# Kernel tuning notes

Hardware: AMD Instinct MI355X
Metric: run time of the kernel (lower is better)

Reference implementation:

```python
import jax, jax.numpy as jnp
import numpy as np

D_MODEL = 1024
D_FFN = 4096
H = 16
D_HEAD = D_MODEL // H
B, L = 2, 2048
EPS = 1e-6


def layer_norm(x, a, b):
    # Matches torch: std is unbiased (ddof=1), and divides by (std + eps)
    mean = jnp.mean(x, axis=-1, keepdims=True)
    var = jnp.sum((x - mean) ** 2, axis=-1, keepdims=True) / (x.shape[-1] - 1)
    std = jnp.sqrt(var)
    return (x - mean) / (std + EPS) * a + b


def setup_inputs() -> dict:
    key = jax.random.key(0)
    ks = jax.random.split(key, 10)
    s = 0.02
    x = jax.random.normal(ks[0], (B, L, D_MODEL), dtype=jnp.float32)
    mask = jnp.tril(jnp.ones((L, L), dtype=jnp.int32))[None, None]  # causal [1,1,L,L]
    return {
        "x": x,
        "mask": mask,
        "Wqkv": jax.random.normal(ks[1], (D_MODEL, 3 * D_MODEL), jnp.float32) * s,
        "bqkv": jnp.zeros((3 * D_MODEL,), jnp.float32),
        "Wo": jax.random.normal(ks[2], (D_MODEL, D_MODEL), jnp.float32) * s,
        "bo": jnp.zeros((D_MODEL,), jnp.float32),
        "W1": jax.random.normal(ks[3], (D_MODEL, D_FFN), jnp.float32) * s,
        "b1": jnp.zeros((D_FFN,), jnp.float32),
        "W2": jax.random.normal(ks[4], (D_FFN, D_MODEL), jnp.float32) * s,
        "b2": jnp.zeros((D_MODEL,), jnp.float32),
        "ln1_a": jnp.ones((D_MODEL,), jnp.float32),
        "ln1_b": jnp.zeros((D_MODEL,), jnp.float32),
        "ln2_a": jnp.ones((D_MODEL,), jnp.float32),
        "ln2_b": jnp.zeros((D_MODEL,), jnp.float32),
    }


def reference(x, mask, Wqkv, bqkv, Wo, bo, W1, b1, W2, b2, ln1_a, ln1_b, ln2_a, ln2_b):
    b, l, d = x.shape
    # --- attention sublayer ---
    qkv = x @ Wqkv + bqkv                                   # [b, l, 3*d]
    qkv = qkv.reshape(b, l, 3, H, D_HEAD)                   # '(three h d)' ordering
    q, k, v = qkv[:, :, 0], qkv[:, :, 1], qkv[:, :, 2]      # each [b, l, h, dh]
    scores = jnp.einsum('bqhd,bkhd->bhqk', q, k) / jnp.sqrt(
        jnp.asarray(D_HEAD, x.dtype))                        # [b, h, lq, lk]
    scores = jnp.where(mask == 0, -jnp.inf, scores)
    p = jax.nn.softmax(scores, axis=-1)
    attn = jnp.einsum('bhqk,bkhd->bqhd', p, v).reshape(b, l, d)
    attn_out = attn @ Wo + bo
    x = layer_norm(x + attn_out, ln1_a, ln1_b)
    # --- MLP sublayer ---
    h = jax.nn.relu(x @ W1 + b1)
    mlp_out = h @ W2 + b2
    return layer_norm(x + mlp_out, ln2_a, ln2_b)
```

## Files before the change

kernel.cpp:

```cpp
#include <hip/hip_runtime.h>

#define D_MODEL 1024
#define D_FFN   4096
#define NH      16
#define DH      64
#define BB      2
#define LL      2048
#define MROWS   (BB * LL)

typedef unsigned short u16;
typedef unsigned int   u32;
typedef short bf16x8 __attribute__((ext_vector_type(8)));
typedef float f32x4  __attribute__((ext_vector_type(4)));

__device__ __forceinline__ float bf2f(u16 u) {
    union { u32 i; float f; } v;
    v.i = ((u32)u) << 16;
    return v.f;
}
__device__ __forceinline__ u16 f2bf(float f) {
    union { float f; u32 i; } v;
    v.f = f;
    u32 x = v.i;
    x += 0x7fffu + ((x >> 16) & 1u);
    return (u16)(x >> 16);
}
__device__ __forceinline__ u32 pack_bf_trunc(float a, float b) {
    return __builtin_amdgcn_perm(__float_as_uint(b), __float_as_uint(a),
                                 0x07060302u);
}

typedef const __attribute__((address_space(1))) u32 gu32;
typedef __attribute__((address_space(3))) u32 lu32;
__device__ __forceinline__ void gload_lds16(const void* g, void* l) {
    __builtin_amdgcn_global_load_lds((gu32*)g, (lu32*)l, 16, 0, 0);
}

__device__ __forceinline__ void wt_tile(
    const float* __restrict__ W, u16* __restrict__ Wt,
    int K, int N, int t, int tid, float* tile )
{
    const int ntiles = N >> 6;
    const int n0 = (t % ntiles) * 64;
    const int k0 = (t / ntiles) * 64;

    int kr = tid >> 4;
    int nc = (tid & 15) * 4;
    #pragma unroll
    for (int p = 0; p < 4; ++p) {
        float4 v = *(const float4*)&W[(size_t)(k0 + kr + p * 16) * N + n0 + nc];
        tile[(kr + p * 16) * 65 + nc + 0] = v.x;
        tile[(kr + p * 16) * 65 + nc + 1] = v.y;
        tile[(kr + p * 16) * 65 + nc + 2] = v.z;
        tile[(kr + p * 16) * 65 + nc + 3] = v.w;
    }
    __syncthreads();

    int nr = tid >> 2;
    int kc = (tid & 3) * 16;
    u16 o[16];
    #pragma unroll
    for (int j = 0; j < 16; ++j) o[j] = f2bf(tile[(kc + j) * 65 + nr]);
    u16* dst = &Wt[(size_t)(n0 + nr) * K + k0 + kc];
    *(uint4*)dst       = *(const uint4*)&o[0];
    *(uint4*)(dst + 8) = *(const uint4*)&o[8];
}

__global__ __launch_bounds__(256) void prep_kernel(
    const float* __restrict__ x,    u16* __restrict__ xb,
    const float* __restrict__ Wqkv, u16* __restrict__ Wqkvt)
{
    __shared__ float tile[64 * 65];
    const int tid = threadIdx.x;
    const int bi  = blockIdx.x;

    if (bi < 2048) {
        int i = bi * 2048 + tid * 8;
        float4 a = *(const float4*)(x + i);
        float4 b = *(const float4*)(x + i + 4);
        u16 o[8] = {f2bf(a.x), f2bf(a.y), f2bf(a.z), f2bf(a.w),
                    f2bf(b.x), f2bf(b.y), f2bf(b.z), f2bf(b.w)};
        *(uint4*)(xb + i) = *(const uint4*)o;
        return;
    }
    wt_tile(Wqkv, Wqkvt, 1024, 3072, bi - 2048, tid, tile);
}

template <int EPI, int RF32, int OF32, int KS>
__global__ __launch_bounds__(256, 4) void gemm_bt_kernel(
    const u16* __restrict__ A, const u16* __restrict__ Bt,
    const float* __restrict__ bias, const void* __restrict__ resv,
    void* __restrict__ out0v, u16* __restrict__ out1, u16* __restrict__ out2,
    int M, int N, int K)
{
    __shared__ u16 sA[128 * 64];
    __shared__ u16 sB[128 * 64];

    const int tid  = threadIdx.x;
    const int lane = tid & 63;
    const int wave = tid >> 6;
    const int wm   = (wave & 1) * 64;
    const int wn   = (wave >> 1) * 64;
    const int quad = lane >> 4;
    const int l16  = lane & 15;

    const int nb  = gridDim.x;
    const int mb  = gridDim.y;
    const int f   = blockIdx.y * nb + blockIdx.x;
    const int xcd = f & 7;
    const int idx = f >> 3;
    const int rn  = nb >> 1;
    const int rm  = mb >> 2;
    const int n0  = ((xcd & 1) * rn + (idx % rn)) * 128;
    const int ym  = (xcd >> 1) * rm + (idx / rn);

    int s, m0;
    if (KS > 1) {
        const int mt = mb / KS;
        s  = ym / mt;
        m0 = (ym % mt) * 128;
    } else {
        s  = 0;
        m0 = ym * 128;
    }
    const int Kseg = K / KS;
    const int kbeg = s * Kseg;

    f32x4 acc[4][4];
    #pragma unroll
    for (int i = 0; i < 4; ++i)
        #pragma unroll
        for (int j = 0; j < 4; ++j)
            acc[i][j] = (f32x4){0.f, 0.f, 0.f, 0.f};

    const u16* Ablk = A  + (size_t)m0 * K;
    const u16* Bblk = Bt + (size_t)n0 * K;

    for (int k0 = kbeg; k0 < kbeg + Kseg; k0 += 64) {
        #pragma unroll
        for (int i = 0; i < 4; ++i) {
            int chunk = (i * 4 + wave) * 64 + lane;
            int r = chunk >> 3;
            int c = (chunk & 7) ^ (r & 7);
            size_t goff = (size_t)r * K + k0 + c * 8;
            gload_lds16(Ablk + goff, &sA[(i * 4 + wave) * 512]);
            gload_lds16(Bblk + goff, &sB[(i * 4 + wave) * 512]);
        }
        __syncthreads();

        #pragma unroll
        for (int ks = 0; ks < 2; ++ks) {
            bf16x8 af[4], bfr[4];
            #pragma unroll
            for (int i = 0; i < 4; ++i) {
                int R = wm + i * 16 + l16;
                int slot = R * 8 + ((ks * 4 + quad) ^ (R & 7));
                af[i] = *(const bf16x8*)&sA[slot * 8];
            }
            #pragma unroll
            for (int j = 0; j < 4; ++j) {
                int R = wn + j * 16 + l16;
                int slot = R * 8 + ((ks * 4 + quad) ^ (R & 7));
                bfr[j] = *(const bf16x8*)&sB[slot * 8];
            }
            #pragma unroll
            for (int i = 0; i < 4; ++i)
                #pragma unroll
                for (int j = 0; j < 4; ++j)
                    acc[i][j] = __builtin_amdgcn_mfma_f32_16x16x32_bf16(
                        af[i], bfr[j], acc[i][j], 0, 0, 0);
        }
        __syncthreads();
    }

    #pragma unroll
    for (int i = 0; i < 4; ++i) {
        int rowb = m0 + wm + i * 16 + quad * 4;
        #pragma unroll
        for (int j = 0; j < 4; ++j) {
            int col = n0 + wn + j * 16 + l16;
            float bv = (EPI == 3) ? 0.f : bias[col];
            #pragma unroll
            for (int r = 0; r < 4; ++r) {
                int rr = rowb + r;
                float v = acc[i][j][r] + bv;
                if (EPI == 0) {
                    int which = col >> 10;
                    int h     = (col >> 6) & 15;
                    int d     = col & 63;
                    int b     = rr >> 11;
                    int l     = rr & 2047;
                    size_t idx2 = ((size_t)(b * NH + h) * LL + l) * DH + d;
                    u16* o0 = (u16*)out0v;
                    if (which == 0)      o0[idx2]   = f2bf(v * 0.18033688f);
                    else if (which == 1) out1[idx2] = f2bf(v);
                    else                 out2[idx2] = f2bf(v);
                } else if (EPI == 3) {
                    ((u16*)out0v)[((size_t)s * M + rr) * N + col] = f2bf(v);
                } else {
                    size_t idx2 = (size_t)rr * N + col;
                    if (EPI == 1) {
                        v += RF32 ? ((const float*)resv)[idx2]
                                  : bf2f(((const u16*)resv)[idx2]);
                    } else {
                        v = v > 0.f ? v : 0.f;
                    }
                    if (OF32) ((float*)out0v)[idx2] = v;
                    else      ((u16*)out0v)[idx2]   = f2bf(v);
                }
            }
        }
    }
}

template <int KS, int RF32, int OF32>
__global__ __launch_bounds__(256) void lnfuse_kernel(
    const u16* __restrict__ P, const float* __restrict__ bias,
    const void* __restrict__ resv,
    const float* __restrict__ ga, const float* __restrict__ gb,
    void* __restrict__ outv)
{
    __shared__ float red[8];
    const int tid  = threadIdx.x;
    const int lane = tid & 63;
    const int wave = tid >> 6;
    const size_t row = blockIdx.x;
    const size_t SL  = (size_t)MROWS * D_MODEL;
    const int c = tid * 4;

    float v0, v1, v2, v3;
    {
        float4 bv = *(const float4*)(bias + c);
        v0 = bv.x; v1 = bv.y; v2 = bv.z; v3 = bv.w;
    }
    #pragma unroll
    for (int s = 0; s < KS; ++s) {
        uint2 p = *(const uint2*)(P + s * SL + row * D_MODEL + c);
        v0 += bf2f((u16)p.x); v1 += bf2f((u16)(p.x >> 16));
        v2 += bf2f((u16)p.y); v3 += bf2f((u16)(p.y >> 16));
    }
    if (RF32) {
        float4 r = *(const float4*)((const float*)resv + row * D_MODEL + c);
        v0 += r.x; v1 += r.y; v2 += r.z; v3 += r.w;
    } else {
        uint2 r = *(const uint2*)((const u16*)resv + row * D_MODEL + c);
        v0 += bf2f((u16)r.x); v1 += bf2f((u16)(r.x >> 16));
        v2 += bf2f((u16)r.y); v3 += bf2f((u16)(r.y >> 16));
    }

    float s_ = v0 + v1 + v2 + v3;
    #pragma unroll
    for (int o = 32; o > 0; o >>= 1) s_ += __shfl_xor(s_, o, 64);
    if (lane == 0) red[wave] = s_;
    __syncthreads();
    float mean = (red[0] + red[1] + red[2] + red[3]) * (1.f / 1024.f);

    float d0 = v0 - mean, d1 = v1 - mean, d2 = v2 - mean, d3 = v3 - mean;
    float q = d0 * d0 + d1 * d1 + d2 * d2 + d3 * d3;
    #pragma unroll
    for (int o = 32; o > 0; o >>= 1) q += __shfl_xor(q, o, 64);
    if (lane == 0) red[4 + wave] = q;
    __syncthreads();
    float var = (red[4] + red[5] + red[6] + red[7]) * (1.f / 1023.f);
    float inv = 1.f / (sqrtf(var) + 1e-6f);

    float y0 = d0 * inv * ga[c + 0] + gb[c + 0];
    float y1 = d1 * inv * ga[c + 1] + gb[c + 1];
    float y2 = d2 * inv * ga[c + 2] + gb[c + 2];
    float y3 = d3 * inv * ga[c + 3] + gb[c + 3];
    if (OF32) {
        float4 y = {y0, y1, y2, y3};
        *(float4*)((float*)outv + row * D_MODEL + c) = y;
    } else {
        ushort4 y = {f2bf(y0), f2bf(y1), f2bf(y2), f2bf(y3)};
        *(ushort4*)((u16*)outv + row * D_MODEL + c) = y;
    }
}

__global__ __launch_bounds__(256) void attn_kernel(
    const u16* __restrict__ Q, const u16* __restrict__ K,
    const u16* __restrict__ V, u16* __restrict__ out,
    const float* __restrict__ Wo, u16* __restrict__ Wot,
    const float* __restrict__ W1, u16* __restrict__ W1t,
    const float* __restrict__ W2, u16* __restrict__ W2t)
{
    __shared__ u16 smem[13824];
    u16* ks = smem;
    u16* vs = smem + 4608;
    u16* ps = smem + 9216;

    const int tid  = threadIdx.x;
    const int bi   = blockIdx.x;

    if (bi >= 1024) {
        float* tile = (float*)smem;
        int t = bi - 1024;
        if (t < 256)       wt_tile(Wo, Wot, 1024, 1024, t,        tid, tile);
        else if (t < 1280) wt_tile(W1, W1t, 1024, 4096, t - 256,  tid, tile);
        else               wt_tile(W2, W2t, 4096, 1024, t - 1280, tid, tile);
        return;
    }

    const int lane = tid & 63;
    const int wave = tid >> 6;
    const int l16  = lane & 15;
    const int quad = lane >> 4;

    const int xcd = bi & 7;
    const int idx = bi >> 3;
    const int bh  = xcd * 4 + (idx & 3);
    const int qt  = 31 - (idx >> 2);
    const int b   = bh >> 4, h = bh & 15;
    const size_t head_off = (size_t)bh * LL * DH;

    const u16* Qh = Q + head_off;
    const u16* Kh = K + head_off;
    const u16* Vh = V + head_off;

    const int base = qt * 64 + wave * 16;
    const int qg   = base + l16;

    const bf16x8 qf0 = *(const bf16x8*)&Qh[(size_t)qg * DH + quad * 8];
    const bf16x8 qf1 = *(const bf16x8*)&Qh[(size_t)qg * DH + 32 + quad * 8];

    float lsum = 0.f;
    f32x4 o[4];
    #pragma unroll
    for (int t = 0; t < 4; ++t) o[t] = (f32x4){0.f, 0.f, 0.f, 0.f};

    u16* psw = ps + wave * 1152;

    const int key = tid >> 2;
    const int kd0 = (tid & 3) * 16;
    const int kp  = tid >> 3;
    const int vd0 = (tid & 7) * 8;

    uint4 kr0, kr1, vr0, vr1;
    {
        const u16* ksrc = Kh + (size_t)key * DH + kd0;
        kr0 = *(const uint4*)ksrc;
        kr1 = *(const uint4*)(ksrc + 8);
        const u16* vsrc = Vh + (size_t)(2 * kp) * DH + vd0;
        vr0 = *(const uint4*)vsrc;
        vr1 = *(const uint4*)(vsrc + DH);
    }

    for (int c = 0; c <= qt; ++c) {
        __syncthreads();
        *(uint4*)&ks[key * 72 + kd0]     = kr0;
        *(uint4*)&ks[key * 72 + kd0 + 8] = kr1;
        {
            const u32* w0 = (const u32*)&vr0;
            const u32* w1 = (const u32*)&vr1;
            #pragma unroll
            for (int e = 0; e < 8; ++e) {
                int d = vd0 + e;
                u32 lo = (w0[e >> 1] >> ((e & 1) * 16)) & 0xffffu;
                u32 hi = (w1[e >> 1] >> ((e & 1) * 16)) & 0xffffu;
                int csw = kp ^ (4 * ((d >> 3) & 7));
                *(u32*)&vs[d * 72 + 2 * csw] = lo | (hi << 16);
            }
        }
        __syncthreads();
        if (c < qt) {
            const u16* ksrc = Kh + (size_t)((c + 1) * 64 + key) * DH + kd0;
            kr0 = *(const uint4*)ksrc;
            kr1 = *(const uint4*)(ksrc + 8);
            const u16* vsrc = Vh + (size_t)((c + 1) * 64 + 2 * kp) * DH + vd0;
            vr0 = *(const uint4*)vsrc;
            vr1 = *(const uint4*)(vsrc + DH);
        }

        f32x4 st[4];
        #pragma unroll
        for (int t = 0; t < 4; ++t) {
            bf16x8 k0 = *(const bf16x8*)&ks[(t * 16 + l16) * 72 + quad * 8];
            bf16x8 k1 = *(const bf16x8*)&ks[(t * 16 + l16) * 72 + 32 + quad * 8];
            f32x4 s = (f32x4){0.f, 0.f, 0.f, 0.f};
            s = __builtin_amdgcn_mfma_f32_16x16x32_bf16(k0, qf0, s, 0, 0, 0);
            s = __builtin_amdgcn_mfma_f32_16x16x32_bf16(k1, qf1, s, 0, 0, 0);
            st[t] = s;
        }

        if (c == qt) {
            #pragma unroll
            for (int t = 0; t < 4; ++t)
                #pragma unroll
                for (int r = 0; r < 4; ++r)
                    if (c * 64 + t * 16 + quad * 4 + r > qg) st[t][r] = -INFINITY;
        }

        {
            float psum = 0.f;
            #pragma unroll
            for (int t = 0; t < 4; ++t) {
                float p0 = exp2f(st[t][0]), p1 = exp2f(st[t][1]);
                float p2 = exp2f(st[t][2]), p3 = exp2f(st[t][3]);
                psum += (p0 + p1) + (p2 + p3);
                uint2 w = {pack_bf_trunc(p0, p1), pack_bf_trunc(p2, p3)};
                *(uint2*)&psw[l16 * 72 + t * 16 + quad * 4] = w;
            }
            psum += __shfl_xor(psum, 16, 64);
            psum += __shfl_xor(psum, 32, 64);
            lsum += psum;
        }

        bf16x8 pf0 = *(const bf16x8*)&psw[l16 * 72 + quad * 8];
        bf16x8 pf1 = *(const bf16x8*)&psw[l16 * 72 + 32 + quad * 8];

        #pragma unroll
        for (int dt = 0; dt < 4; ++dt) {
            int d  = dt * 16 + l16;
            int sw = 4 * ((d >> 3) & 7);
            bf16x8 vf0 = *(const bf16x8*)&vs[d * 72 + 2 * ((quad * 4) ^ sw)];
            bf16x8 vf1 = *(const bf16x8*)&vs[d * 72 + 2 * ((16 + quad * 4) ^ sw)];
            o[dt] = __builtin_amdgcn_mfma_f32_16x16x32_bf16(pf0, vf0, o[dt], 0, 0, 0);
            o[dt] = __builtin_amdgcn_mfma_f32_16x16x32_bf16(pf1, vf1, o[dt], 0, 0, 0);
        }
    }

    {
        float i0 = 1.f / __shfl(lsum, quad * 4 + 0, 64);
        float i1 = 1.f / __shfl(lsum, quad * 4 + 1, 64);
        float i2 = 1.f / __shfl(lsum, quad * 4 + 2, 64);
        float i3 = 1.f / __shfl(lsum, quad * 4 + 3, 64);
        #pragma unroll
        for (int dt = 0; dt < 4; ++dt) {
            size_t col = h * DH + dt * 16 + l16;
            size_t r0  = ((size_t)b * LL + base + quad * 4) * D_MODEL + col;
            out[r0]               = f2bf(o[dt][0] * i0);
            out[r0 + D_MODEL]     = f2bf(o[dt][1] * i1);
            out[r0 + 2 * D_MODEL] = f2bf(o[dt][2] * i2);
            out[r0 + 3 * D_MODEL] = f2bf(o[dt][3] * i3);
        }
    }
}

extern "C" void kernel_launch(void* const* d_in, const int* in_sizes, int n_in,
                              void* d_out, int out_size, void* d_ws, size_t ws_size,
                              hipStream_t stream)
{
    const float* x    = (const float*)d_in[0];
    const float* Wqkv = (const float*)d_in[2];
    const float* bqkv = (const float*)d_in[3];
    const float* Wo   = (const float*)d_in[4];
    const float* bo   = (const float*)d_in[5];
    const float* W1   = (const float*)d_in[6];
    const float* b1   = (const float*)d_in[7];
    const float* W2   = (const float*)d_in[8];
    const float* b2   = (const float*)d_in[9];
    const float* ln1a = (const float*)d_in[10];
    const float* ln1b = (const float*)d_in[11];
    const float* ln2a = (const float*)d_in[12];
    const float* ln2b = (const float*)d_in[13];

    char* ws = (char*)d_ws;
    const size_t HSZ = (size_t)BB * NH * LL * DH;
    u16*   Qp    = (u16*)ws;
    u16*   Kp    = Qp + HSZ;
    u16*   Vp    = Kp + HSZ;
    u16*   attn  = Vp + HSZ;
    u16*   hbuf  = (u16*)ws;
    u16*   xb    = (u16*)(ws + 33554432);
    u16*   x1    = (u16*)(ws + 50331648);
    u16*   Wqkvt = (u16*)(ws + 58720256);
    u16*   Wot   = (u16*)(ws + 65011712);
    u16*   W1t   = (u16*)(ws + 67108864);
    u16*   W2t   = (u16*)(ws + 75497472);
    u16*   Pbuf  = (u16*)(ws + 83886080);

    dim3 blk(256);

    prep_kernel<<<dim3(2816), blk, 0, stream>>>(x, xb, Wqkv, Wqkvt);

    gemm_bt_kernel<0,0,0,1><<<dim3(24, 32), blk, 0, stream>>>(
        xb, Wqkvt, bqkv, nullptr, Qp, Kp, Vp, MROWS, 3 * D_MODEL, D_MODEL);
    attn_kernel<<<dim3(3328), blk, 0, stream>>>(
        Qp, Kp, Vp, attn, Wo, Wot, W1, W1t, W2, W2t);
    gemm_bt_kernel<3,0,0,2><<<dim3(8, 64), blk, 0, stream>>>(
        attn, Wot, bo, nullptr, Pbuf, nullptr, nullptr, MROWS, D_MODEL, D_MODEL);
    lnfuse_kernel<2,1,0><<<dim3(MROWS), blk, 0, stream>>>(
        Pbuf, bo, x, ln1a, ln1b, x1);
    gemm_bt_kernel<2,0,0,1><<<dim3(32, 32), blk, 0, stream>>>(
        x1, W1t, b1, nullptr, hbuf, nullptr, nullptr, MROWS, D_FFN, D_MODEL);
    gemm_bt_kernel<3,0,0,4><<<dim3(8, 128), blk, 0, stream>>>(
        hbuf, W2t, b2, nullptr, Pbuf, nullptr, nullptr, MROWS, D_MODEL, D_FFN);
    lnfuse_kernel<4,0,1><<<dim3(MROWS), blk, 0, stream>>>(
        Pbuf, b2, x1, ln2a, ln2b, d_out);
}
```

Measured before the change: 319.1 us.

## Emit V transposed from QKV GEMM epilogue to simplify attention V staging

The QKV GEMM epilogue now writes V in a [b,h,d,l] transposed layout, staging the tile through shared memory so global stores are 16-byte vectors along the sequence dimension. The attention kernel then loads V rows already transposed and stores them into shared memory with two vector writes, replacing the per-element shuffle and scalar stores. This moves the transpose cost from every attention tile iteration to a single pass in the GEMM epilogue. It adds an extra shared-memory round trip and barrier in the V-producing GEMM blocks.

Result: no change. 318.2 us (-0.3%).

```diff
diff --git a/kernel.cpp b/kernel.cpp
--- a/kernel.cpp
+++ b/kernel.cpp
@@ -93,8 +93,9 @@
     void* __restrict__ out0v, u16* __restrict__ out1, u16* __restrict__ out2,
     int M, int N, int K)
 {
-    __shared__ u16 sA[128 * 64];
-    __shared__ u16 sB[128 * 64];
+    __shared__ u16 smem[16384];
+    u16* sA = smem;
+    u16* sB = smem + 8192;
 
     const int tid  = threadIdx.x;
     const int lane = tid & 63;
@@ -173,6 +174,39 @@
         __syncthreads();
     }
 
+    if (EPI == 0 && n0 >= 2 * D_MODEL) {
+        u16* tile = smem;
+        #pragma unroll
+        for (int i = 0; i < 4; ++i) {
+            int rl = wm + i * 16 + quad * 4;
+            #pragma unroll
+            for (int j = 0; j < 4; ++j) {
+                int cl = wn + j * 16 + l16;
+                float bv = bias[n0 + cl];
+                int sx = 8 * (cl & 15);
+                #pragma unroll
+                for (int r = 0; r < 4; ++r)
+                    tile[cl * 128 + ((rl + r) ^ sx)] = f2bf(acc[i][j][r] + bv);
+            }
+        }
+        __syncthreads();
+        int cl  = tid >> 1;
+        int rb  = (tid & 1) * 64;
+        int col = n0 + cl;
+        int h   = (col >> 6) & 15;
+        int d   = col & 63;
+        int b   = m0 >> 11;
+        int l0  = (m0 & 2047) + rb;
+        int sx  = 8 * (cl & 15);
+        u16* dst = out2 + ((size_t)(b * NH + h) * DH + d) * LL + l0;
+        #pragma unroll
+        for (int u = 0; u < 8; ++u) {
+            uint4 q = *(const uint4*)&tile[cl * 128 + ((rb + 8 * u) ^ sx)];
+            *(uint4*)(dst + 8 * u) = q;
+        }
+        return;
+    }
+
     #pragma unroll
     for (int i = 0; i < 4; ++i) {
         int rowb = m0 + wm + i * 16 + quad * 4;
@@ -185,16 +219,14 @@
                 int rr = rowb + r;
                 float v = acc[i][j][r] + bv;
                 if (EPI == 0) {
-                    int which = col >> 10;
                     int h     = (col >> 6) & 15;
                     int d     = col & 63;
                     int b     = rr >> 11;
                     int l     = rr & 2047;
                     size_t idx2 = ((size_t)(b * NH + h) * LL + l) * DH + d;
                     u16* o0 = (u16*)out0v;
-                    if (which == 0)      o0[idx2]   = f2bf(v * 0.18033688f);
-                    else if (which == 1) out1[idx2] = f2bf(v);
-                    else                 out2[idx2] = f2bf(v);
+                    if (col < D_MODEL)  o0[idx2]   = f2bf(v * 0.18033688f);
+                    else                out1[idx2] = f2bf(v);
                 } else if (EPI == 3) {
                     ((u16*)out0v)[((size_t)s * M + rr) * N + col] = f2bf(v);
                 } else {
@@ -332,43 +364,37 @@
 
     const int key = tid >> 2;
     const int kd0 = (tid & 3) * 16;
-    const int kp  = tid >> 3;
-    const int vd0 = (tid & 7) * 8;
+
+    const int vC    = 4 * ((key >> 3) & 7);
+    const int vbase = (kd0 >> 1) ^ (vC & 24);
+    const int vofA  = vbase + (vC & 4);
+    const int vofB  = vbase + ((vC & 4) ^ 4);
+    u32* vs32 = (u32*)vs;
 
     uint4 kr0, kr1, vr0, vr1;
     {
         const u16* ksrc = Kh + (size_t)key * DH + kd0;
         kr0 = *(const uint4*)ksrc;
         kr1 = *(const uint4*)(ksrc + 8);
-        const u16* vsrc = Vh + (size_t)(2 * kp) * DH + vd0;
+        const u16* vsrc = Vh + (size_t)key * LL + kd0;
         vr0 = *(const uint4*)vsrc;
-        vr1 = *(const uint4*)(vsrc + DH);
+        vr1 = *(const uint4*)(vsrc + 8);
     }
 
     for (int c = 0; c <= qt; ++c) {
         __syncthreads();
         *(uint4*)&ks[key * 72 + kd0]     = kr0;
         *(uint4*)&ks[key * 72 + kd0 + 8] = kr1;
-        {
-            const u32* w0 = (const u32*)&vr0;
-            const u32* w1 = (const u32*)&vr1;
-            #pragma unroll
-            for (int e = 0; e < 8; ++e) {
-                int d = vd0 + e;
-                u32 lo = (w0[e >> 1] >> ((e & 1) * 16)) & 0xffffu;
-                u32 hi = (w1[e >> 1] >> ((e & 1) * 16)) & 0xffffu;
-                int csw = kp ^ (4 * ((d >> 3) & 7));
-                *(u32*)&vs[d * 72 + 2 * csw] = lo | (hi << 16);
-            }
-        }
+        *(uint4*)&vs32[key * 36 + vofA]  = vr0;
+        *(uint4*)&vs32[key * 36 + vofB]  = vr1;
         __syncthreads();
         if (c < qt) {
             const u16* ksrc = Kh + (size_t)((c + 1) * 64 + key) * DH + kd0;
             kr0 = *(const uint4*)ksrc;
             kr1 = *(const uint4*)(ksrc + 8);
-            const u16* vsrc = Vh + (size_t)((c + 1) * 64 + 2 * kp) * DH + vd0;
+            const u16* vsrc = Vh + (size_t)key * LL + (c + 1) * 64 + kd0;
             vr0 = *(const uint4*)vsrc;
-            vr1 = *(const uint4*)(vsrc + DH);
+            vr1 = *(const uint4*)(vsrc + 8);
         }
 
         f32x4 st[4];
```
